# Kernel optimization log

Measured on AMD Instinct MI355X. Metric: run time of the kernel, lower is better.

Reference implementation:

```python
import jax, jax.numpy as jnp
import numpy as np

OUT_CHN, IN_CHN, K = 256, 256, 3
STRIDE, PADDING = 1, 1

def binary_activation(x):
    # STE: forward = sign(x), backward = piecewise-polynomial surrogate out3
    m1 = (x < -1).astype(x.dtype)
    m2 = (x < 0).astype(x.dtype)
    m3 = (x < 1).astype(x.dtype)
    out1 = -1.0 * m1 + (x * x + 2 * x) * (1 - m1)
    out2 = out1 * m2 + (-x * x + 2 * x) * (1 - m2)
    out3 = out2 * m3 + 1.0 * (1 - m3)
    return jax.lax.stop_gradient(jnp.sign(x)) - jax.lax.stop_gradient(out3) + out3

def setup_inputs() -> dict:
    key = jax.random.key(0)
    kx, kw = jax.random.split(key)
    x = jax.random.normal(kx, (32, IN_CHN, 56, 56), dtype=jnp.float32)
    # weights stored flat [N,1] as in the torch module, scaled by 0.001
    weights = jax.random.uniform(kw, (OUT_CHN * IN_CHN * K * K, 1), dtype=jnp.float32) * 0.001
    return {"x": x, "weights": weights}

def reference(x, weights):
    w = weights.reshape(OUT_CHN, IN_CHN, K, K)
    # STE for weights: forward = sign(w), backward = clamp(w,-1,1)
    clipped = jnp.clip(w, -1.0, 1.0)
    bw = jax.lax.stop_gradient(jnp.sign(w)) - jax.lax.stop_gradient(clipped) + clipped
    bx = binary_activation(x)
    y = jax.lax.conv_general_dilated(
        bx, bw,
        window_strides=(STRIDE, STRIDE),
        padding=[(PADDING, PADDING), (PADDING, PADDING)],
        dimension_numbers=("NCHW", "OIHW", "NCHW"),
    )
    return y
```

## Files before the change

### kernel.cpp

```cpp
#include <hip/hip_runtime.h>
#include <stdint.h>

#define N_BATCH 32
#define CHN     256
#define HW      56
#define HP      58

#define XPAD_CELLS (N_BATCH * HP * 2 * HP)
#define XPAD_U32   (XPAD_CELLS * 4)

__global__ __launch_bounds__(256) void prep_kernel(const float* __restrict__ x,
                                                   const float* __restrict__ wsrc,
                                                   uint32_t* __restrict__ xpad,
                                                   uint32_t* __restrict__ wbits,
                                                   int* __restrict__ wpop) {
    __shared__ int part[9][4];
    int bid  = blockIdx.x;
    int t    = threadIdx.x;
    int lane = t & 63;

    if (bid < 784) {
        int tid = bid * 256 + t;
        int n   = tid / 6272;
        int rem = tid - n * 6272;
        int hf  = rem / 3136;
        int pq  = rem - hf * 3136;

        const float* src = x + ((size_t)(n * 256 + hf * 128)) * 3136 + pq;
        uint32_t b0 = 0, b1 = 0, b2 = 0, b3 = 0;
#pragma unroll
        for (int g = 0; g < 8; g++) {
            float v[16];
#pragma unroll
            for (int i = 0; i < 16; i++) v[i] = src[(size_t)(g * 16 + i) * 3136];
#pragma unroll
            for (int i = 0; i < 16; i++) {
                int c = g * 16 + i;
                uint32_t b = v[i] > 0.0f ? 1u : 0u;
                if ((c >> 5) == 0) b0 |= b << (c & 31);
                else if ((c >> 5) == 1) b1 |= b << (c & 31);
                else if ((c >> 5) == 2) b2 |= b << (c & 31);
                else b3 |= b << (c & 31);
            }
        }
        int h = pq / 56;
        int w = pq - h * 56;
        uint32_t cell = ((uint32_t)(n * HP + h + 1) * 2 + hf) * HP + (w + 1);
        ((uint4*)xpad)[cell] = make_uint4(b0, b1, b2, b3);
    } else if (bid < 841) {
        int u = (bid - 784) * 256 + t;
        if (u < 14592) {
            int p = u / 228;
            int e = u - p * 228;
            int n = p >> 1, h = p & 1;
            int hp, wp;
            if (e < 58)       { hp = 0;       wp = e;       }
            else if (e < 116) { hp = 57;      wp = e - 58;  }
            else if (e < 172) { hp = e - 115; wp = 0;       }
            else              { hp = e - 171; wp = 57;      }
            uint32_t cell = ((uint32_t)(n * HP + hp) * 2 + h) * HP + wp;
            ((uint4*)xpad)[cell] = make_uint4(0u, 0u, 0u, 0u);
        }
    } else {
        int o  = bid - 841;
        int wv = t >> 6;
        const float* p = wsrc + ((size_t)o * 256 + t) * 9;
        float v[9];
#pragma unroll
        for (int tap = 0; tap < 9; tap++) v[tap] = p[tap];
#pragma unroll
        for (int tap = 0; tap < 9; tap++) {
            unsigned long long m = __ballot(v[tap] > 0.0f);
            if (lane == 0) {
                wbits[(size_t)(o * 9 + tap) * 8 + 2 * wv]     = (uint32_t)m;
                wbits[(size_t)(o * 9 + tap) * 8 + 2 * wv + 1] = (uint32_t)(m >> 32);
                part[tap][wv] = __builtin_popcountll(m);
            }
        }
        __syncthreads();
        if (t < 9) wpop[o * 9 + t] = part[t][0] + part[t][1] + part[t][2] + part[t][3];
    }
}

__global__ __launch_bounds__(256, 2)
void conv_kernel(const uint32_t* __restrict__ xpad,
                 const uint32_t* __restrict__ wbits,
                 const int* __restrict__ wpop,
                 float* __restrict__ out) {
    __shared__ uint4 sx[3 * 2 * HP];
    __shared__ short obuf[4 * 64 * 57];

    int t    = threadIdx.x;
    int lane = t & 63;
    int wv   = t >> 6;
    int h    = blockIdx.x;
    int n    = blockIdx.y;

    const uint4* xg = (const uint4*)xpad + ((size_t)n * HP + h) * (2 * HP);
    for (int i = t; i < 3 * 2 * HP; i += 256) sx[i] = xg[i];

    int o = wv * 64 + lane;
    const uint4* wsrc4 = (const uint4*)(wbits + (size_t)o * 72);
    uint4 W4[18];
#pragma unroll
    for (int i = 0; i < 18; i++) W4[i] = wsrc4[i];

    const int* wpa = wpop + (size_t)o * 9;
    int pa[9];
#pragma unroll
    for (int i = 0; i < 9; i++) pa[i] = wpa[i];

    __syncthreads();

    short* ob  = obuf + wv * (64 * 57) + lane * 57;
    bool hedge = (h == 0) | (h == 55);

#pragma unroll 2
    for (int w = 0; w < 56; w++) {
        const uint4* cb = sx + w;
        int a0 = 0, a1 = 0, a2 = 0, a3 = 0;
#pragma unroll
        for (int r = 0; r < 3; r++)
#pragma unroll
            for (int dw = 0; dw < 3; dw++)
#pragma unroll
                for (int hf = 0; hf < 2; hf++) {
                    uint4 Xc = cb[(r * 2 + hf) * HP + dw];
                    uint4 Wc = W4[(r * 3 + dw) * 2 + hf];
                    a0 += __builtin_popcount(Xc.x ^ Wc.x);
                    a1 += __builtin_popcount(Xc.y ^ Wc.y);
                    a2 += __builtin_popcount(Xc.z ^ Wc.z);
                    a3 += __builtin_popcount(Xc.w ^ Wc.w);
                }
        int va = 2304 - 2 * ((a0 + a1) + (a2 + a3));
        if (hedge | (w == 0) | (w == 55)) {
            int ca = 0;
#pragma unroll
            for (int dh = 0; dh < 3; dh++)
#pragma unroll
                for (int dw = 0; dw < 3; dw++)
                    if ((unsigned)(h + dh - 1) >= 56u || (unsigned)(w + dw - 1) >= 56u)
                        ca += 256 - 2 * pa[dh * 3 + dw];
            va -= ca;
        }
        ob[w] = (short)va;
    }

    if (lane < 56) {
        const short* obw = obuf + wv * (64 * 57);
        float* orow = out + (((size_t)n * 256 + wv * 64) * 56 + h) * 56 + lane;
#pragma unroll 8
        for (int o2 = 0; o2 < 64; o2++)
            orow[(size_t)o2 * 3136] = (float)obw[o2 * 57 + lane];
    }
}

extern "C" void kernel_launch(void* const* d_in, const int* in_sizes, int n_in,
                              void* d_out, int out_size, void* d_ws, size_t ws_size,
                              hipStream_t stream) {
    const float* x    = (const float*)d_in[0];
    const float* wsrc = (const float*)d_in[1];
    float* out = (float*)d_out;

    uint32_t* xpad  = (uint32_t*)d_ws;
    uint32_t* wbits = xpad + XPAD_U32;
    int*      wpop  = (int*)(wbits + 256 * 9 * 8);

    prep_kernel<<<1097, 256, 0, stream>>>(x, wsrc, xpad, wbits, wpop);
    conv_kernel<<<dim3(HW, N_BATCH), 256, 0, stream>>>(xpad, wbits, wpop, out);
}
```

Measured before the change: 319.3 us.

## Register-block two output channels per thread and split width across waves

Each thread now computes two output channels (o and o+128) over half the row width instead of one channel over the full width. Each LDS load of an input cell is reused for two weight sets, halving LDS traffic per popcount. Edge-correction popcounts for both channels are packed into one register, and a block barrier is added before the store phase because waves now write each other's rows. This doubles weight registers per thread, which may lower occupancy or cause spills, and the width loop is no longer unrolled.

```diff
diff --git a/kernel.cpp b/kernel.cpp
--- a/kernel.cpp
+++ b/kernel.cpp
@@ -88,66 +88,88 @@
                  const int* __restrict__ wpop,
                  float* __restrict__ out) {
     __shared__ uint4 sx[3 * 2 * HP];
-    __shared__ short obuf[4 * 64 * 57];
+    __shared__ short obuf[256 * 57];
 
     int t    = threadIdx.x;
     int lane = t & 63;
     int wv   = t >> 6;
+    int og   = wv & 1;
+    int pH   = wv >> 1;
     int h    = blockIdx.x;
     int n    = blockIdx.y;
 
     const uint4* xg = (const uint4*)xpad + ((size_t)n * HP + h) * (2 * HP);
     for (int i = t; i < 3 * 2 * HP; i += 256) sx[i] = xg[i];
 
-    int o = wv * 64 + lane;
-    const uint4* wsrc4 = (const uint4*)(wbits + (size_t)o * 72);
-    uint4 W4[18];
+    int o1 = og * 64 + lane;
+    const uint4* w1p = (const uint4*)(wbits + (size_t)o1 * 72);
+    const uint4* w2p = (const uint4*)(wbits + (size_t)(o1 + 128) * 72);
+    uint4 WA[18], WB[18];
 #pragma unroll
-    for (int i = 0; i < 18; i++) W4[i] = wsrc4[i];
+    for (int i = 0; i < 18; i++) WA[i] = w1p[i];
+#pragma unroll
+    for (int i = 0; i < 18; i++) WB[i] = w2p[i];
 
-    const int* wpa = wpop + (size_t)o * 9;
-    int pa[9];
+    const int* pp1 = wpop + (size_t)o1 * 9;
+    const int* pp2 = wpop + (size_t)(o1 + 128) * 9;
+    uint32_t papack[9];
 #pragma unroll
-    for (int i = 0; i < 9; i++) pa[i] = wpa[i];
+    for (int i = 0; i < 9; i++)
+        papack[i] = (uint32_t)pp1[i] | ((uint32_t)pp2[i] << 16);
 
     __syncthreads();
 
-    short* ob  = obuf + wv * (64 * 57) + lane * 57;
+    short* ob1 = obuf + o1 * 57;
+    short* ob2 = obuf + (o1 + 128) * 57;
     bool hedge = (h == 0) | (h == 55);
+    int w0 = pH * 28;
 
-#pragma unroll 2
-    for (int w = 0; w < 56; w++) {
+#pragma unroll 1
+    for (int wi = 0; wi < 28; wi++) {
+        int w = w0 + wi;
         const uint4* cb = sx + w;
         int a0 = 0, a1 = 0, a2 = 0, a3 = 0;
+        int b0 = 0, b1 = 0, b2 = 0, b3 = 0;
 #pragma unroll
-        for (int r = 0; r < 3; r++)
+        for (int dw = 0; dw < 3; dw++)
 #pragma unroll
-            for (int dw = 0; dw < 3; dw++)
-#pragma unroll
-                for (int hf = 0; hf < 2; hf++) {
-                    uint4 Xc = cb[(r * 2 + hf) * HP + dw];
-                    uint4 Wc = W4[(r * 3 + dw) * 2 + hf];
-                    a0 += __builtin_popcount(Xc.x ^ Wc.x);
-                    a1 += __builtin_popcount(Xc.y ^ Wc.y);
-                    a2 += __builtin_popcount(Xc.z ^ Wc.z);
-                    a3 += __builtin_popcount(Xc.w ^ Wc.w);
-                }
+            for (int rr = 0; rr < 6; rr++) {
+                uint4 xc = cb[rr * HP + dw];
+                uint4 wa = WA[((rr >> 1) * 3 + dw) * 2 + (rr & 1)];
+                uint4 wb = WB[((rr >> 1) * 3 + dw) * 2 + (rr & 1)];
+                a0 += __builtin_popcount(xc.x ^ wa.x);
+                a1 += __builtin_popcount(xc.y ^ wa.y);
+                a2 += __builtin_popcount(xc.z ^ wa.z);
+                a3 += __builtin_popcount(xc.w ^ wa.w);
+                b0 += __builtin_popcount(xc.x ^ wb.x);
+                b1 += __builtin_popcount(xc.y ^ wb.y);
+                b2 += __builtin_popcount(xc.z ^ wb.z);
+                b3 += __builtin_popcount(xc.w ^ wb.w);
+            }
         int va = 2304 - 2 * ((a0 + a1) + (a2 + a3));
+        int vb = 2304 - 2 * ((b0 + b1) + (b2 + b3));
         if (hedge | (w == 0) | (w == 55)) {
-            int ca = 0;
+            int ca = 0, cc = 0;
 #pragma unroll
             for (int dh = 0; dh < 3; dh++)
 #pragma unroll
                 for (int dw = 0; dw < 3; dw++)
-                    if ((unsigned)(h + dh - 1) >= 56u || (unsigned)(w + dw - 1) >= 56u)
-                        ca += 256 - 2 * pa[dh * 3 + dw];
+                    if ((unsigned)(h + dh - 1) >= 56u || (unsigned)(w + dw - 1) >= 56u) {
+                        uint32_t pk = papack[dh * 3 + dw];
+                        ca += 256 - 2 * (int)(pk & 0xffffu);
+                        cc += 256 - 2 * (int)(pk >> 16);
+                    }
             va -= ca;
+            vb -= cc;
         }
-        ob[w] = (short)va;
+        ob1[w] = (short)va;
+        ob2[w] = (short)vb;
     }
 
+    __syncthreads();
+
     if (lane < 56) {
-        const short* obw = obuf + wv * (64 * 57);
+        const short* obw = obuf + (wv * 64) * 57;
         float* orow = out + (((size_t)n * 256 + wv * 64) * 56 + h) * 56 + lane;
 #pragma unroll 8
         for (int o2 = 0; o2 < 64; o2++)
```

After: 307.6 us. 1.04x faster.

## Split conv work across channel halves and output groups, read inputs via scalar loads

Applied to the files above, without the earlier changes.

The conv kernel now splits the 256 input channels into two halves, one per pair of waves, and splits the output channels across a new grid z dimension of 2. This doubles the block count and halves the per-thread weight registers. Input rows are read directly from global memory through a wave-uniform (readfirstlane) base address instead of being staged in shared memory. The two channel-half partial sums are combined through LDS after a barrier. In exchange, each input row is fetched twice (once per output half), and the loop is no longer unrolled.

```diff
diff --git a/kernel.cpp b/kernel.cpp
--- a/kernel.cpp
+++ b/kernel.cpp
@@ -87,71 +87,77 @@
                  const uint32_t* __restrict__ wbits,
                  const int* __restrict__ wpop,
                  float* __restrict__ out) {
-    __shared__ uint4 sx[3 * 2 * HP];
-    __shared__ short obuf[4 * 64 * 57];
+    __shared__ short obuf[2][128][57];
 
     int t    = threadIdx.x;
     int lane = t & 63;
     int wv   = t >> 6;
+    int hf   = wv >> 1;
+    int og   = wv & 1;
     int h    = blockIdx.x;
     int n    = blockIdx.y;
+    int oh   = blockIdx.z;
 
-    const uint4* xg = (const uint4*)xpad + ((size_t)n * HP + h) * (2 * HP);
-    for (int i = t; i < 3 * 2 * HP; i += 256) sx[i] = xg[i];
+    int ol = og * 64 + lane;
+    int o  = oh * 128 + ol;
+    uint4 W[9];
+#pragma unroll
+    for (int tap = 0; tap < 9; tap++)
+        W[tap] = *(const uint4*)(wbits + ((size_t)o * 9 + tap) * 8 + hf * 4);
 
-    int o = wv * 64 + lane;
-    const uint4* wsrc4 = (const uint4*)(wbits + (size_t)o * 72);
-    uint4 W4[18];
+    int pa[9];
+    if (hf == 0) {
+        const int* wpa = wpop + (size_t)o * 9;
 #pragma unroll
-    for (int i = 0; i < 18; i++) W4[i] = wsrc4[i];
+        for (int i = 0; i < 9; i++) pa[i] = wpa[i];
+    }
 
-    const int* wpa = wpop + (size_t)o * 9;
-    int pa[9];
-#pragma unroll
-    for (int i = 0; i < 9; i++) pa[i] = wpa[i];
+    int rowbase = __builtin_amdgcn_readfirstlane(((n * HP + h) * 2 + hf) * HP);
+    const uint4* xr = (const uint4*)xpad + rowbase;
 
-    __syncthreads();
-
-    short* ob  = obuf + wv * (64 * 57) + lane * 57;
+    short* ob  = &obuf[hf][ol][0];
     bool hedge = (h == 0) | (h == 55);
 
-#pragma unroll 2
+#pragma unroll 1
     for (int w = 0; w < 56; w++) {
-        const uint4* cb = sx + w;
         int a0 = 0, a1 = 0, a2 = 0, a3 = 0;
 #pragma unroll
         for (int r = 0; r < 3; r++)
 #pragma unroll
-            for (int dw = 0; dw < 3; dw++)
+            for (int dw = 0; dw < 3; dw++) {
+                uint4 xc = xr[r * (2 * HP) + w + dw];
+                uint4 wc = W[r * 3 + dw];
+                a0 += __builtin_popcount(xc.x ^ wc.x);
+                a1 += __builtin_popcount(xc.y ^ wc.y);
+                a2 += __builtin_popcount(xc.z ^ wc.z);
+                a3 += __builtin_popcount(xc.w ^ wc.w);
+            }
+        int vp = 1152 - 2 * ((a0 + a1) + (a2 + a3));
+        if (hf == 0) {
+            if (hedge | (w == 0) | (w == 55)) {
+                int ca = 0;
 #pragma unroll
-                for (int hf = 0; hf < 2; hf++) {
-                    uint4 Xc = cb[(r * 2 + hf) * HP + dw];
-                    uint4 Wc = W4[(r * 3 + dw) * 2 + hf];
-                    a0 += __builtin_popcount(Xc.x ^ Wc.x);
-                    a1 += __builtin_popcount(Xc.y ^ Wc.y);
-                    a2 += __builtin_popcount(Xc.z ^ Wc.z);
-                    a3 += __builtin_popcount(Xc.w ^ Wc.w);
-                }
-        int va = 2304 - 2 * ((a0 + a1) + (a2 + a3));
-        if (hedge | (w == 0) | (w == 55)) {
-            int ca = 0;
+                for (int dh = 0; dh < 3; dh++)
 #pragma unroll
-            for (int dh = 0; dh < 3; dh++)
-#pragma unroll
-                for (int dw = 0; dw < 3; dw++)
-                    if ((unsigned)(h + dh - 1) >= 56u || (unsigned)(w + dw - 1) >= 56u)
-                        ca += 256 - 2 * pa[dh * 3 + dw];
-            va -= ca;
+                    for (int dw = 0; dw < 3; dw++)
+                        if ((unsigned)(h + dh - 1) >= 56u || (unsigned)(w + dw - 1) >= 56u)
+                            ca += 256 - 2 * pa[dh * 3 + dw];
+                vp -= ca;
+            }
         }
-        ob[w] = (short)va;
+        ob[w] = (short)vp;
     }
 
+    __syncthreads();
+
     if (lane < 56) {
-        const short* obw = obuf + wv * (64 * 57);
-        float* orow = out + (((size_t)n * 256 + wv * 64) * 56 + h) * 56 + lane;
+        int base = wv * 32;
+        float* orow = out + (((size_t)n * 256 + oh * 128 + base) * 56 + h) * 56 + lane;
 #pragma unroll 8
-        for (int o2 = 0; o2 < 64; o2++)
-            orow[(size_t)o2 * 3136] = (float)obw[o2 * 57 + lane];
+        for (int i = 0; i < 32; i++) {
+            int v = (int)obuf[0][base + i][lane] + (int)obuf[1][base + i][lane];
+            orow[(size_t)i * 3136] = (float)v;
+        }
     }
 }
 
@@ -167,5 +173,5 @@
     int*      wpop  = (int*)(wbits + 256 * 9 * 8);
 
     prep_kernel<<<1097, 256, 0, stream>>>(x, wsrc, xpad, wbits, wpop);
-    conv_kernel<<<dim3(HW, N_BATCH), 256, 0, stream>>>(xpad, wbits, wpop, out);
+    conv_kernel<<<dim3(HW, N_BATCH, 2), 256, 0, stream>>>(xpad, wbits, wpop, out);
 }
```

New measurement: 312.5 us. -2.1%, faster.
